# Kernel optimization log

Hardware: AMD Instinct MI355X
Metric: run time of the kernel (lower is better)

Reference implementation:

```python
import jax, jax.numpy as jnp
import numpy as np

B, T, I, H = 512, 256, 7, 64


def setup_inputs() -> dict:
    key = jax.random.key(0)
    d = {
        "x": jax.random.normal(jax.random.fold_in(key, 0), (B, T, I), jnp.float32),
        "C": jnp.zeros((B, H, H), jnp.float32),
        "n": jnp.zeros((B, H, H), jnp.float32),
    }
    for j, nm in enumerate(["Wq", "Wk", "Wv", "Wi", "Wf", "Wo"]):
        d[nm] = jax.random.normal(jax.random.fold_in(key, j + 1), (H, I), jnp.float32)
        d["b" + nm[1]] = jnp.zeros((H,), jnp.float32)
    return d


def reference(x, C, n, Wq, Wk, Wv, Wi, Wf, Wo, bq, bk, bv, bi, bf, bo):
    # x: [B,T,I]; C,n: [B,H,H] matrix memory / normalizer state
    Hdim = Wq.shape[0]
    scale = 1.0 / jnp.sqrt(jnp.asarray(Hdim, x.dtype))
    q = jnp.einsum('bti,hi->bth', x, Wq) + bq
    k = scale * (jnp.einsum('bti,hi->bth', x, Wk) + bk)
    v = jnp.einsum('bti,hi->bth', x, Wv) + bv
    i = jnp.exp(jnp.einsum('bti,hi->bth', x, Wi) + bi)
    f = jax.nn.sigmoid(jnp.einsum('bti,hi->bth', x, Wf) + bf)
    o = jax.nn.sigmoid(jnp.einsum('bti,hi->bth', x, Wo) + bo)
    # time-major for scan: each gate [T,B,H]
    gates = tuple(jnp.swapaxes(g, 0, 1) for g in (q, k, v, i, f, o))

    def step(carry, g):
        C, n = carry                      # [B,H,H]
        qt, kt, vt, it, ft, ot = g        # [B,H]
        ik = it * kt                      # [B,H]
        # torch: C = f*C + i*outer(v,k)  -> C[r,c] = f[c]*C[r,c] + i[c]*v[r]*k[c]
        C = ft[:, None, :] * C + ik[:, None, :] * vt[:, :, None]
        # torch: n = f*n + i*k (broadcast over rows)
        n = ft[:, None, :] * n + ik[:, None, :]
        num = jnp.einsum('brc,bc->br', C, qt)          # C @ q
        den = jnp.einsum('brc,br->bc', n, qt)          # n.T @ q
        h = ot * jnp.tanh(num / jnp.maximum(den, 1.0))
        return (C, n), h

    (C, n), hs = jax.lax.scan(step, (C, n), gates)
    return jnp.swapaxes(hs, 0, 1), C, n  # h: [B,T,H]
```

## Files before the change

### kernel.cpp

```cpp
#include <hip/hip_runtime.h>
#include <math.h>

#define B_ 512
#define T_ 256
#define I_ 7
#define H_ 64
#define L_ 16
#define NCH_ (T_ / L_)
#define L2E 1.44269504089f
#define GUARD2 (-21.64f)

typedef short bf16x8 __attribute__((ext_vector_type(8)));
typedef short short4v __attribute__((ext_vector_type(4)));
typedef float f32x4 __attribute__((ext_vector_type(4)));

__device__ __forceinline__ unsigned short f2bf(float f) {
  unsigned u = __float_as_uint(f);
  u += 0x7fff + ((u >> 16) & 1);
  return (unsigned short)(u >> 16);
}
__device__ __forceinline__ float ex2(float x) { return __builtin_amdgcn_exp2f(x); }
__device__ __forceinline__ float lg2(float x) { return __builtin_amdgcn_logf(x); }
__device__ __forceinline__ float logsig2(float a2) {
  return (a2 < GUARD2) ? a2 : -lg2(1.f + ex2(-a2));
}
__device__ __forceinline__ float sig2(float a2) {
  return __fdividef(1.f, 1.f + ex2(-a2));
}

#define PRODUCE_IKV(BUF, XP) do {                                             \
  float ls8[8], ik8[8];                                                       \
  unsigned short kv[8], vv[8];                                                \
  _Pragma("unroll") for (int tt = 0; tt < 8; ++tt) {                          \
    const int t = tb + tt;                                                    \
    float xs[7];                                                              \
    _Pragma("unroll") for (int jj = 0; jj < 7; ++jj) xs[jj] = (XP)[t * 7 + jj]; \
    float fp = bF2, ip = bI2, kp = bK, vp = bV;                               \
    _Pragma("unroll") for (int jj = 0; jj < 7; ++jj) {                        \
      fp = fmaf(xs[jj], wf2[jj], fp); ip = fmaf(xs[jj], wi2[jj], ip);         \
      kp = fmaf(xs[jj], wk[jj], kp);  vp = fmaf(xs[jj], wv[jj], vp);          \
    }                                                                         \
    ls8[tt] = logsig2(fp);                                                    \
    const float ikv = ex2(ip) * kp * 0.125f;                                  \
    ik8[tt] = ikv;                                                            \
    sIK[BUF][t][lane] = ikv;                                                  \
    vv[tt] = f2bf(vp);                                                        \
  }                                                                           \
  _Pragma("unroll") for (int tt = 1; tt < 8; ++tt) ls8[tt] += ls8[tt - 1];    \
  _Pragma("unroll") for (int tt = 0; tt < 8; ++tt) {                          \
    const float e = (tb == 0) ? (ls8[7] - ls8[tt]) : (-ls8[tt]);              \
    const float u = ik8[tt] * ex2(e);                                         \
    kv[tt] = f2bf(u);                                                         \
    sKt[BUF][tb + tt][lane] = kv[tt];                                         \
  }                                                                           \
  { short4v p0 = {(short)kv[0], (short)kv[1], (short)kv[2], (short)kv[3]};    \
    short4v p1 = {(short)kv[4], (short)kv[5], (short)kv[6], (short)kv[7]};    \
    *(short4v*)&sKnT[BUF][lane][tb]     = p0;                                 \
    *(short4v*)&sKnT[BUF][lane][tb + 4] = p1;                                 \
    short4v q0 = {(short)vv[0], (short)vv[1], (short)vv[2], (short)vv[3]};    \
    short4v q1 = {(short)vv[4], (short)vv[5], (short)vv[6], (short)vv[7]};    \
    *(short4v*)&sVT[BUF][lane][tb]     = q0;                                  \
    *(short4v*)&sVT[BUF][lane][tb + 4] = q1; }                                \
} while (0)

#define PRODUCE_F(BUF, XP) do {                                               \
  float ls[16];                                                               \
  _Pragma("unroll") for (int t = 0; t < 16; ++t) {                            \
    float xs[7];                                                              \
    _Pragma("unroll") for (int jj = 0; jj < 7; ++jj) xs[jj] = (XP)[t * 7 + jj]; \
    float fp = bF2;                                                           \
    _Pragma("unroll") for (int jj = 0; jj < 7; ++jj) fp = fmaf(xs[jj], wf2[jj], fp); \
    const float ena = ex2(-fp);                                               \
    sFs[BUF][t][lane] = __fdividef(1.f, 1.f + ena);                           \
    ls[t] = (fp < GUARD2) ? fp : -lg2(1.f + ena);                             \
  }                                                                           \
  _Pragma("unroll") for (int t = 1; t < 16; ++t) ls[t] += ls[t - 1];          \
  sEM[BUF][lane]   = ex2(ls[7]);                                              \
  sFtot[BUF][lane] = ex2(ls[15]);                                             \
  sCF[BUF][lane]   = ex2(ls[15] - ls[7]);                                     \
  { const int tq = lane & 15;                                                 \
    float Sqv = wqs[7];                                                       \
    _Pragma("unroll") for (int jj = 0; jj < 7; ++jj)                          \
      Sqv = fmaf((XP)[tq * 7 + jj], wqs[jj], Sqv);                            \
    if (lane < 16) sSq[BUF][tq] = Sqv; }                                      \
} while (0)

#define PRODUCE_Q(BUF, XP) do {                                               \
  float qv[16], ls[16];                                                       \
  _Pragma("unroll") for (int t = 0; t < 16; ++t) {                            \
    float xs[7];                                                              \
    _Pragma("unroll") for (int jj = 0; jj < 7; ++jj) xs[jj] = (XP)[t * 7 + jj]; \
    float qq = bQ, fp = bF2;                                                  \
    _Pragma("unroll") for (int jj = 0; jj < 7; ++jj) {                        \
      qq = fmaf(xs[jj], wq[jj], qq); fp = fmaf(xs[jj], wf2[jj], fp);          \
    }                                                                         \
    qv[t] = qq;                                                               \
    ls[t] = logsig2(fp);                                                      \
  }                                                                           \
  _Pragma("unroll") for (int t = 1; t < 16; ++t) ls[t] += ls[t - 1];          \
  const float m = ls[7];                                                      \
  _Pragma("unroll") for (int t = 0; t < 16; ++t)                              \
    sQt[BUF][t][lane] = f2bf(qv[t] * ex2(ls[t] - m));                         \
} while (0)

__global__ __launch_bounds__(512, 4) void mlstm_ws3(
    const float* __restrict__ x,
    const float* __restrict__ Cin,
    const float* __restrict__ nin,
    const float* __restrict__ Wq, const float* __restrict__ bq,
    const float* __restrict__ Wk, const float* __restrict__ bk,
    const float* __restrict__ Wv, const float* __restrict__ bv,
    const float* __restrict__ Wi, const float* __restrict__ bi,
    const float* __restrict__ Wf, const float* __restrict__ bf,
    const float* __restrict__ Wo, const float* __restrict__ bo,
    float* __restrict__ hout, float* __restrict__ Cout, float* __restrict__ nout)
{
  const int b    = blockIdx.x;
  const int tid  = threadIdx.x;
  const int lane = tid & 63;
  const int w    = __builtin_amdgcn_readfirstlane(tid >> 6);
  const int quad = lane >> 4;
  const int sl   = lane & 15;

  __shared__ __align__(16) unsigned short sQt[2][L_][72];
  __shared__ __align__(16) unsigned short sKt[2][L_][72];
  __shared__ __align__(16) unsigned short sVT[2][H_][40];
  __shared__ __align__(16) unsigned short sKnT[2][H_][40];
  __shared__ __align__(16) unsigned short sS[4][L_][40];
  __shared__ __align__(16) unsigned short sC0[H_][72];
  __shared__ float sFs[2][L_][H_];
  __shared__ float sIK[2][L_][H_];
  __shared__ float sSq[2][L_];
  __shared__ float sEM[2][H_];
  __shared__ float sFtot[2][H_];
  __shared__ float sCF[2][H_];
  __shared__ float sNv[H_];

  for (int idx = tid; idx < 1024; idx += 512) {
    const int bu = idx >> 9, r = (idx >> 3) & 63, d = idx & 7;
    ((unsigned*)sVT)[(bu * 64 + r) * 20 + 8 + d]  = 0;
    ((unsigned*)sKnT)[(bu * 64 + r) * 20 + 8 + d] = 0;
  }
  for (int idx = tid; idx < 1280; idx += 512) ((unsigned*)sS)[idx] = 0;

  const float* __restrict__ xb = x + (size_t)b * T_ * I_;

  if (w < 4) {
    const int c0 = 16 * w + sl;
    float wOl[7];
#pragma unroll
    for (int jj = 0; jj < 7; ++jj) wOl[jj] = Wo[c0 * 7 + jj] * L2E;
    const float bO2 = bo[c0] * L2E;
    f32x4 Cacc[4];
#pragma unroll
    for (int ct = 0; ct < 4; ++ct)
#pragma unroll
      for (int reg = 0; reg < 4; ++reg)
        Cacc[ct][reg] =
            Cin[(size_t)b * H_ * H_ + (size_t)(16 * w + 4 * quad + reg) * H_ + 16 * ct + sl];
    float nv = nin[(size_t)b * H_ * H_ + c0];
    __syncthreads();
    for (int j = 0; j < NCH_; ++j) {
      const int p = j & 1;
      const float* xc = xb + (size_t)j * L_ * I_;
      float den4[4];
#pragma unroll
      for (int t = 0; t < 16; ++t) {
        const float fs  = sFs[p][t][c0];
        const float ikv = sIK[p][t][c0];
        nv = fmaf(fs, nv, ikv);
        if ((t >> 2) == quad) den4[t & 3] = nv;
      }
      float idn[4], oo[4];
#pragma unroll
      for (int r2 = 0; r2 < 4; ++r2) {
        const int t = 4 * quad + r2;
        idn[r2] = __fdividef(1.f, fmaxf(den4[r2] * sSq[p][t], 1.f));
        float op = bO2;
#pragma unroll
        for (int jj = 0; jj < 7; ++jj) op = fmaf(xc[t * 7 + jj], wOl[jj], op);
        oo[r2] = sig2(op);
      }
      const bf16x8 aQ0 = *(const bf16x8*)&sQt[p][sl][8 * quad];
      const bf16x8 aQ1 = *(const bf16x8*)&sQt[p][sl][32 + 8 * quad];
      const bf16x8 bK0 = *(const bf16x8*)&sKt[p][sl][8 * quad];
      const bf16x8 bK1 = *(const bf16x8*)&sKt[p][sl][32 + 8 * quad];
      f32x4 Sv = {0.f, 0.f, 0.f, 0.f};
      Sv = __builtin_amdgcn_mfma_f32_16x16x32_bf16(aQ0, bK0, Sv, 0, 0, 0);
      Sv = __builtin_amdgcn_mfma_f32_16x16x32_bf16(aQ1, bK1, Sv, 0, 0, 0);
#pragma unroll
      for (int reg = 0; reg < 4; ++reg) {
        const int t = 4 * quad + reg;
        sS[w][t][sl] = f2bf((sl <= t) ? Sv[reg] : 0.f);
      }
      const bf16x8 aV = *(const bf16x8*)&sVT[p][c0][8 * quad];
      f32x4 G[4];
      float ftA[4], cfA[4];
#pragma unroll
      for (int ct = 0; ct < 4; ++ct) {
        const int cc = 16 * ct + sl;
        const float emv = sEM[p][cc];
        ftA[ct] = sFtot[p][cc];
        cfA[ct] = sCF[p][cc];
#pragma unroll
        for (int reg = 0; reg < 4; ++reg)
          sC0[16 * w + 4 * quad + reg][cc] = f2bf(Cacc[ct][reg] * emv);
        const bf16x8 bKn = *(const bf16x8*)&sKnT[p][cc][8 * quad];
        f32x4 z = {0.f, 0.f, 0.f, 0.f};
        G[ct] = __builtin_amdgcn_mfma_f32_16x16x32_bf16(aV, bKn, z, 0, 0, 0);
      }
      const bf16x8 bC0a = *(const bf16x8*)&sC0[c0][8 * quad];
      const bf16x8 bC0b = *(const bf16x8*)&sC0[c0][32 + 8 * quad];
      const bf16x8 aS   = *(const bf16x8*)&sS[w][sl][8 * quad];
      f32x4 Num = {0.f, 0.f, 0.f, 0.f};
      Num = __builtin_amdgcn_mfma_f32_16x16x32_bf16(aQ0, bC0a, Num, 0, 0, 0);
      Num = __builtin_amdgcn_mfma_f32_16x16x32_bf16(aQ1, bC0b, Num, 0, 0, 0);
      Num = __builtin_amdgcn_mfma_f32_16x16x32_bf16(aS, aV, Num, 0, 0, 0);
#pragma unroll
      for (int reg = 0; reg < 4; ++reg) {
        const int t = 4 * quad + reg;
        const float y = Num[reg] * idn[reg];
        const float e = ex2(y * 2.88539008178f);
        const float th = 1.f - __fdividef(2.f, e + 1.f);
        hout[(size_t)b * T_ * H_ + (size_t)(j * L_ + t) * H_ + c0] = oo[reg] * th;
      }
#pragma unroll
      for (int ct = 0; ct < 4; ++ct) Cacc[ct] = Cacc[ct] * ftA[ct] + G[ct] * cfA[ct];
      __syncthreads();
    }
#pragma unroll
    for (int ct = 0; ct < 4; ++ct)
#pragma unroll
      for (int reg = 0; reg < 4; ++reg)
        Cout[(size_t)b * H_ * H_ + (size_t)(16 * w + 4 * quad + reg) * H_ + 16 * ct + sl] =
            Cacc[ct][reg];
    if (quad == 0) sNv[c0] = nv;
  } else if (w == 4 || w == 5) {
    const int tb = (w == 4) ? 0 : 8;
    float wi2[7], wk[7], wf2[7], wv[7];
#pragma unroll
    for (int jj = 0; jj < 7; ++jj) {
      wi2[jj] = Wi[lane * 7 + jj] * L2E;
      wk[jj]  = Wk[lane * 7 + jj];
      wf2[jj] = Wf[lane * 7 + jj] * L2E;
      wv[jj]  = Wv[lane * 7 + jj];
    }
    const float bI2 = bi[lane] * L2E, bK = bk[lane], bF2 = bf[lane] * L2E, bV = bv[lane];
    PRODUCE_IKV(0, xb);
    __syncthreads();
    for (int j = 0; j < NCH_; ++j) {
      if (j + 1 < NCH_) {
        const int pn = (j + 1) & 1;
        const float* xn = xb + (size_t)(j + 1) * L_ * I_;
        if (pn) PRODUCE_IKV(1, xn); else PRODUCE_IKV(0, xn);
      }
      __syncthreads();
    }
  } else if (w == 6) {
    float wf2[7], wqs[8];
#pragma unroll
    for (int jj = 0; jj < 7; ++jj) wf2[jj] = Wf[lane * 7 + jj] * L2E;
    const float bF2 = bf[lane] * L2E;
#pragma unroll
    for (int jj = 0; jj < 7; ++jj) {
      float s = 0.f;
      for (int r = 0; r < H_; ++r) s += Wq[r * 7 + jj];
      wqs[jj] = s;
    }
    {
      float s = 0.f;
      for (int r = 0; r < H_; ++r) s += bq[r];
      wqs[7] = s;
    }
    PRODUCE_F(0, xb);
    __syncthreads();
    for (int j = 0; j < NCH_; ++j) {
      if (j + 1 < NCH_) {
        const int pn = (j + 1) & 1;
        const float* xn = xb + (size_t)(j + 1) * L_ * I_;
        if (pn) PRODUCE_F(1, xn); else PRODUCE_F(0, xn);
      }
      __syncthreads();
    }
  } else {
    float wq[7], wf2[7];
#pragma unroll
    for (int jj = 0; jj < 7; ++jj) {
      wq[jj]  = Wq[lane * 7 + jj];
      wf2[jj] = Wf[lane * 7 + jj] * L2E;
    }
    const float bQ = bq[lane], bF2 = bf[lane] * L2E;
    PRODUCE_Q(0, xb);
    __syncthreads();
    for (int j = 0; j < NCH_; ++j) {
      if (j + 1 < NCH_) {
        const int pn = (j + 1) & 1;
        const float* xn = xb + (size_t)(j + 1) * L_ * I_;
        if (pn) PRODUCE_Q(1, xn); else PRODUCE_Q(0, xn);
      }
      __syncthreads();
    }
  }

  __syncthreads();
  {
    const float nvv = sNv[lane];
#pragma unroll
    for (int k = 0; k < 8; ++k)
      nout[(size_t)b * H_ * H_ + (size_t)(8 * w + k) * H_ + lane] = nvv;
  }
}

extern "C" void kernel_launch(void* const* d_in, const int* in_sizes, int n_in,
                              void* d_out, int out_size, void* d_ws, size_t ws_size,
                              hipStream_t stream) {
  const float* xp  = (const float*)d_in[0];
  const float* Cp  = (const float*)d_in[1];
  const float* np_ = (const float*)d_in[2];

  const float* W[6];
  const float* Bv[6];
  if (n_in >= 15 && in_sizes[4] == 64) {
    for (int g = 0; g < 6; ++g) {
      W[g]  = (const float*)d_in[3 + 2 * g];
      Bv[g] = (const float*)d_in[4 + 2 * g];
    }
  } else {
    for (int g = 0; g < 6; ++g) {
      W[g]  = (const float*)d_in[3 + g];
      Bv[g] = (const float*)d_in[9 + g];
    }
  }

  float* hout = (float*)d_out;
  float* Cout = hout + (size_t)B_ * T_ * H_;
  float* nout = Cout + (size_t)B_ * H_ * H_;

  mlstm_ws3<<<dim3(B_), dim3(512), 0, stream>>>(
      xp, Cp, np_,
      W[0], Bv[0], W[1], Bv[1], W[2], Bv[2],
      W[3], Bv[3], W[4], Bv[4], W[5], Bv[5],
      hout, Cout, nout);
}
```

Before: 155.4 us.

## Split each batch across two row-half blocks with fewer producer warps

Each batch element now runs as two 256-thread blocks that each own 32 rows of the C state, which doubles the grid and shrinks per-block shared memory. The producer roles are consolidated: one warp computes i, k and f plus the decay factors, and another computes q together with the summed q row. V projection moves into the consumer warps, and the forget gate is rebuilt from stored log-sigmoids. Each half-block recomputes the full k/f/q projections, so that work is duplicated in exchange for more parallelism and occupancy.

```diff
diff --git a/kernel.cpp b/kernel.cpp
--- a/kernel.cpp
+++ b/kernel.cpp
@@ -28,82 +28,79 @@
   return __fdividef(1.f, 1.f + ex2(-a2));
 }
 
-#define PRODUCE_IKV(BUF, XP) do {                                             \
-  float ls8[8], ik8[8];                                                       \
-  unsigned short kv[8], vv[8];                                                \
-  _Pragma("unroll") for (int tt = 0; tt < 8; ++tt) {                          \
-    const int t = tb + tt;                                                    \
-    float xs[7];                                                              \
-    _Pragma("unroll") for (int jj = 0; jj < 7; ++jj) xs[jj] = (XP)[t * 7 + jj]; \
-    float fp = bF2, ip = bI2, kp = bK, vp = bV;                               \
-    _Pragma("unroll") for (int jj = 0; jj < 7; ++jj) {                        \
-      fp = fmaf(xs[jj], wf2[jj], fp); ip = fmaf(xs[jj], wi2[jj], ip);         \
-      kp = fmaf(xs[jj], wk[jj], kp);  vp = fmaf(xs[jj], wv[jj], vp);          \
-    }                                                                         \
-    ls8[tt] = logsig2(fp);                                                    \
-    const float ikv = ex2(ip) * kp * 0.125f;                                  \
-    ik8[tt] = ikv;                                                            \
-    sIK[BUF][t][lane] = ikv;                                                  \
-    vv[tt] = f2bf(vp);                                                        \
-  }                                                                           \
-  _Pragma("unroll") for (int tt = 1; tt < 8; ++tt) ls8[tt] += ls8[tt - 1];    \
-  _Pragma("unroll") for (int tt = 0; tt < 8; ++tt) {                          \
-    const float e = (tb == 0) ? (ls8[7] - ls8[tt]) : (-ls8[tt]);              \
-    const float u = ik8[tt] * ex2(e);                                         \
-    kv[tt] = f2bf(u);                                                         \
-    sKt[BUF][tb + tt][lane] = kv[tt];                                         \
-  }                                                                           \
-  { short4v p0 = {(short)kv[0], (short)kv[1], (short)kv[2], (short)kv[3]};    \
-    short4v p1 = {(short)kv[4], (short)kv[5], (short)kv[6], (short)kv[7]};    \
-    *(short4v*)&sKnT[BUF][lane][tb]     = p0;                                 \
-    *(short4v*)&sKnT[BUF][lane][tb + 4] = p1;                                 \
-    short4v q0 = {(short)vv[0], (short)vv[1], (short)vv[2], (short)vv[3]};    \
-    short4v q1 = {(short)vv[4], (short)vv[5], (short)vv[6], (short)vv[7]};    \
-    *(short4v*)&sVT[BUF][lane][tb]     = q0;                                  \
-    *(short4v*)&sVT[BUF][lane][tb + 4] = q1; }                                \
+#define CONS_V(BUF, XP) do {                                                  \
+  unsigned short vv[4];                                                       \
+  _Pragma("unroll") for (int i2 = 0; i2 < 4; ++i2) {                          \
+    const int t = 4 * quad + i2;                                              \
+    float vp = bV;                                                            \
+    _Pragma("unroll") for (int jj = 0; jj < 7; ++jj)                          \
+      vp = fmaf((XP)[t * 7 + jj], wVl[jj], vp);                               \
+    vv[i2] = f2bf(vp);                                                        \
+  }                                                                           \
+  short4v pk = {(short)vv[0], (short)vv[1], (short)vv[2], (short)vv[3]};      \
+  *(short4v*)&sVT[BUF][16 * w + sl][4 * quad] = pk;                           \
 } while (0)
 
-#define PRODUCE_F(BUF, XP) do {                                               \
-  float ls[16];                                                               \
+#define PROD_IKF(BUF, XP) do {                                                \
+  float cl[16], ikv[16];                                                      \
   _Pragma("unroll") for (int t = 0; t < 16; ++t) {                            \
     float xs[7];                                                              \
     _Pragma("unroll") for (int jj = 0; jj < 7; ++jj) xs[jj] = (XP)[t * 7 + jj]; \
-    float fp = bF2;                                                           \
-    _Pragma("unroll") for (int jj = 0; jj < 7; ++jj) fp = fmaf(xs[jj], wf2[jj], fp); \
-    const float ena = ex2(-fp);                                               \
-    sFs[BUF][t][lane] = __fdividef(1.f, 1.f + ena);                           \
-    ls[t] = (fp < GUARD2) ? fp : -lg2(1.f + ena);                             \
-  }                                                                           \
-  _Pragma("unroll") for (int t = 1; t < 16; ++t) ls[t] += ls[t - 1];          \
-  sEM[BUF][lane]   = ex2(ls[7]);                                              \
-  sFtot[BUF][lane] = ex2(ls[15]);                                             \
-  sCF[BUF][lane]   = ex2(ls[15] - ls[7]);                                     \
-  { const int tq = lane & 15;                                                 \
-    float Sqv = wqs[7];                                                       \
-    _Pragma("unroll") for (int jj = 0; jj < 7; ++jj)                          \
-      Sqv = fmaf((XP)[tq * 7 + jj], wqs[jj], Sqv);                            \
-    if (lane < 16) sSq[BUF][tq] = Sqv; }                                      \
+    float fp = bF2, ip = bI2, kp = bK;                                        \
+    _Pragma("unroll") for (int jj = 0; jj < 7; ++jj) {                        \
+      fp = fmaf(xs[jj], wf2[jj], fp);                                         \
+      ip = fmaf(xs[jj], wi2[jj], ip);                                         \
+      kp = fmaf(xs[jj], wk[jj], kp);                                          \
+    }                                                                         \
+    const float ls = logsig2(fp);                                             \
+    cl[t] = ls;                                                               \
+    const float ik = ex2(ip) * kp * 0.125f;                                   \
+    ikv[t] = ik;                                                              \
+    if (oh) { sIK[BUF][t][lc2] = ik; sLs[BUF][t][lc2] = ls; }                 \
+  }                                                                           \
+  _Pragma("unroll") for (int t = 1; t < 16; ++t) cl[t] += cl[t - 1];          \
+  const float m = cl[7];                                                      \
+  sEM[BUF][lane] = ex2(m);                                                    \
+  sCF[BUF][lane] = ex2(cl[15] - m);                                           \
+  unsigned short kvv[16];                                                     \
+  _Pragma("unroll") for (int t = 0; t < 16; ++t) {                            \
+    const float u = ikv[t] * ex2(m - cl[t]);                                  \
+    kvv[t] = f2bf(u);                                                         \
+    sKt[BUF][t][lane] = kvv[t];                                               \
+  }                                                                           \
+  _Pragma("unroll") for (int g = 0; g < 4; ++g) {                             \
+    short4v pk = {(short)kvv[4 * g], (short)kvv[4 * g + 1],                   \
+                  (short)kvv[4 * g + 2], (short)kvv[4 * g + 3]};              \
+    *(short4v*)&sKnT[BUF][lane][4 * g] = pk;                                  \
+  }                                                                           \
 } while (0)
 
-#define PRODUCE_Q(BUF, XP) do {                                               \
-  float qv[16], ls[16];                                                       \
+#define PROD_Q(BUF, XP) do {                                                  \
+  float qv[16], cl[16];                                                       \
   _Pragma("unroll") for (int t = 0; t < 16; ++t) {                            \
     float xs[7];                                                              \
     _Pragma("unroll") for (int jj = 0; jj < 7; ++jj) xs[jj] = (XP)[t * 7 + jj]; \
     float qq = bQ, fp = bF2;                                                  \
     _Pragma("unroll") for (int jj = 0; jj < 7; ++jj) {                        \
-      qq = fmaf(xs[jj], wq[jj], qq); fp = fmaf(xs[jj], wf2[jj], fp);          \
+      qq = fmaf(xs[jj], wq[jj], qq);                                          \
+      fp = fmaf(xs[jj], wf2[jj], fp);                                         \
     }                                                                         \
     qv[t] = qq;                                                               \
-    ls[t] = logsig2(fp);                                                      \
-  }                                                                           \
-  _Pragma("unroll") for (int t = 1; t < 16; ++t) ls[t] += ls[t - 1];          \
-  const float m = ls[7];                                                      \
+    cl[t] = logsig2(fp);                                                      \
+  }                                                                           \
+  _Pragma("unroll") for (int t = 1; t < 16; ++t) cl[t] += cl[t - 1];          \
+  const float m = cl[7];                                                      \
   _Pragma("unroll") for (int t = 0; t < 16; ++t)                              \
-    sQt[BUF][t][lane] = f2bf(qv[t] * ex2(ls[t] - m));                         \
+    sQt[BUF][t][lane] = f2bf(qv[t] * ex2(cl[t] - m));                         \
+  if (lane < 16) {                                                            \
+    float Sqv = wqs[7];                                                       \
+    _Pragma("unroll") for (int jj = 0; jj < 7; ++jj)                          \
+      Sqv = fmaf((XP)[lane * 7 + jj], wqs[jj], Sqv);                          \
+    sSq[BUF][lane] = Sqv;                                                     \
+  }                                                                           \
 } while (0)
 
-__global__ __launch_bounds__(512, 4) void mlstm_ws3(
+__global__ __launch_bounds__(256, 4) void mlstm_rs(
     const float* __restrict__ x,
     const float* __restrict__ Cin,
     const float* __restrict__ nin,
@@ -115,7 +112,10 @@
     const float* __restrict__ Wo, const float* __restrict__ bo,
     float* __restrict__ hout, float* __restrict__ Cout, float* __restrict__ nout)
 {
-  const int b    = blockIdx.x;
+  const int bb   = blockIdx.x;
+  const int b    = bb >> 1;
+  const int half = bb & 1;
+  const int rbase = half << 5;
   const int tid  = threadIdx.x;
   const int lane = tid & 63;
   const int w    = __builtin_amdgcn_readfirstlane(tid >> 6);
@@ -124,62 +124,59 @@
 
   __shared__ __align__(16) unsigned short sQt[2][L_][72];
   __shared__ __align__(16) unsigned short sKt[2][L_][72];
-  __shared__ __align__(16) unsigned short sVT[2][H_][40];
   __shared__ __align__(16) unsigned short sKnT[2][H_][40];
-  __shared__ __align__(16) unsigned short sS[4][L_][40];
-  __shared__ __align__(16) unsigned short sC0[H_][72];
-  __shared__ float sFs[2][L_][H_];
-  __shared__ float sIK[2][L_][H_];
+  __shared__ __align__(16) unsigned short sVT[2][32][40];
+  __shared__ __align__(16) unsigned short sS[2][L_][32];
+  __shared__ __align__(16) unsigned short sC0[32][72];
+  __shared__ float sLs[2][L_][32];
+  __shared__ float sIK[2][L_][32];
   __shared__ float sSq[2][L_];
   __shared__ float sEM[2][H_];
-  __shared__ float sFtot[2][H_];
   __shared__ float sCF[2][H_];
-  __shared__ float sNv[H_];
-
-  for (int idx = tid; idx < 1024; idx += 512) {
-    const int bu = idx >> 9, r = (idx >> 3) & 63, d = idx & 7;
-    ((unsigned*)sVT)[(bu * 64 + r) * 20 + 8 + d]  = 0;
-    ((unsigned*)sKnT)[(bu * 64 + r) * 20 + 8 + d] = 0;
-  }
-  for (int idx = tid; idx < 1280; idx += 512) ((unsigned*)sS)[idx] = 0;
+  __shared__ float sNv[32];
+
+  for (int idx = tid; idx < 1024; idx += 256) {
+    const int r = idx >> 3, d = idx & 7;
+    ((unsigned*)sKnT)[r * 20 + 8 + d] = 0;
+  }
+  for (int idx = tid; idx < 512; idx += 256) {
+    const int r = idx >> 3, d = idx & 7;
+    ((unsigned*)sVT)[r * 20 + 8 + d] = 0;
+  }
+  for (int idx = tid; idx < 512; idx += 256) ((unsigned*)sS)[idx] = 0;
 
   const float* __restrict__ xb = x + (size_t)b * T_ * I_;
 
-  if (w < 4) {
-    const int c0 = 16 * w + sl;
-    float wOl[7];
-#pragma unroll
-    for (int jj = 0; jj < 7; ++jj) wOl[jj] = Wo[c0 * 7 + jj] * L2E;
-    const float bO2 = bo[c0] * L2E;
+  if (w < 2) {
+    const int lc  = 16 * w + sl;
+    const int c0g = rbase + lc;
+    float wOl[7], wVl[7];
+#pragma unroll
+    for (int jj = 0; jj < 7; ++jj) {
+      wOl[jj] = Wo[c0g * 7 + jj] * L2E;
+      wVl[jj] = Wv[c0g * 7 + jj];
+    }
+    const float bO2 = bo[c0g] * L2E, bV = bv[c0g];
     f32x4 Cacc[4];
 #pragma unroll
     for (int ct = 0; ct < 4; ++ct)
 #pragma unroll
       for (int reg = 0; reg < 4; ++reg)
-        Cacc[ct][reg] =
-            Cin[(size_t)b * H_ * H_ + (size_t)(16 * w + 4 * quad + reg) * H_ + 16 * ct + sl];
-    float nv = nin[(size_t)b * H_ * H_ + c0];
+        Cacc[ct][reg] = Cin[(size_t)b * H_ * H_ +
+                            (size_t)(rbase + 16 * w + 4 * quad + reg) * H_ + 16 * ct + sl];
+    float nv = nin[(size_t)b * H_ * H_ + c0g];
+    CONS_V(0, xb);
     __syncthreads();
     for (int j = 0; j < NCH_; ++j) {
-      const int p = j & 1;
+      const int p = j & 1, pn = p ^ 1;
       const float* xc = xb + (size_t)j * L_ * I_;
+      const float* xn = xc + L_ * I_;
       float den4[4];
 #pragma unroll
       for (int t = 0; t < 16; ++t) {
-        const float fs  = sFs[p][t][c0];
-        const float ikv = sIK[p][t][c0];
-        nv = fmaf(fs, nv, ikv);
+        const float fs = ex2(sLs[p][t][lc]);
+        nv = fmaf(fs, nv, sIK[p][t][lc]);
         if ((t >> 2) == quad) den4[t & 3] = nv;
-      }
-      float idn[4], oo[4];
-#pragma unroll
-      for (int r2 = 0; r2 < 4; ++r2) {
-        const int t = 4 * quad + r2;
-        idn[r2] = __fdividef(1.f, fmaxf(den4[r2] * sSq[p][t], 1.f));
-        float op = bO2;
-#pragma unroll
-        for (int jj = 0; jj < 7; ++jj) op = fmaf(xc[t * 7 + jj], wOl[jj], op);
-        oo[r2] = sig2(op);
       }
       const bf16x8 aQ0 = *(const bf16x8*)&sQt[p][sl][8 * quad];
       const bf16x8 aQ1 = *(const bf16x8*)&sQt[p][sl][32 + 8 * quad];
@@ -188,20 +185,30 @@
       f32x4 Sv = {0.f, 0.f, 0.f, 0.f};
       Sv = __builtin_amdgcn_mfma_f32_16x16x32_bf16(aQ0, bK0, Sv, 0, 0, 0);
       Sv = __builtin_amdgcn_mfma_f32_16x16x32_bf16(aQ1, bK1, Sv, 0, 0, 0);
+      float idn[4], oo[4];
+#pragma unroll
+      for (int r2 = 0; r2 < 4; ++r2) {
+        const int t = 4 * quad + r2;
+        idn[r2] = __fdividef(1.f, fmaxf(den4[r2] * sSq[p][t], 1.f));
+        float op = bO2;
+#pragma unroll
+        for (int jj = 0; jj < 7; ++jj) op = fmaf(xc[t * 7 + jj], wOl[jj], op);
+        oo[r2] = sig2(op);
+      }
 #pragma unroll
       for (int reg = 0; reg < 4; ++reg) {
         const int t = 4 * quad + reg;
         sS[w][t][sl] = f2bf((sl <= t) ? Sv[reg] : 0.f);
       }
-      const bf16x8 aV = *(const bf16x8*)&sVT[p][c0][8 * quad];
+      const bf16x8 aV = *(const bf16x8*)&sVT[p][16 * w + sl][8 * quad];
       f32x4 G[4];
       float ftA[4], cfA[4];
 #pragma unroll
       for (int ct = 0; ct < 4; ++ct) {
         const int cc = 16 * ct + sl;
         const float emv = sEM[p][cc];
-        ftA[ct] = sFtot[p][cc];
         cfA[ct] = sCF[p][cc];
+        ftA[ct] = emv * cfA[ct];
 #pragma unroll
         for (int reg = 0; reg < 4; ++reg)
           sC0[16 * w + 4 * quad + reg][cc] = f2bf(Cacc[ct][reg] * emv);
@@ -209,8 +216,9 @@
         f32x4 z = {0.f, 0.f, 0.f, 0.f};
         G[ct] = __builtin_amdgcn_mfma_f32_16x16x32_bf16(aV, bKn, z, 0, 0, 0);
       }
-      const bf16x8 bC0a = *(const bf16x8*)&sC0[c0][8 * quad];
-      const bf16x8 bC0b = *(const bf16x8*)&sC0[c0][32 + 8 * quad];
+      if (j + 1 < NCH_) CONS_V(pn, xn);
+      const bf16x8 bC0a = *(const bf16x8*)&sC0[16 * w + sl][8 * quad];
+      const bf16x8 bC0b = *(const bf16x8*)&sC0[16 * w + sl][32 + 8 * quad];
       const bf16x8 aS   = *(const bf16x8*)&sS[w][sl][8 * quad];
       f32x4 Num = {0.f, 0.f, 0.f, 0.f};
       Num = __builtin_amdgcn_mfma_f32_16x16x32_bf16(aQ0, bC0a, Num, 0, 0, 0);
@@ -222,7 +230,7 @@
         const float y = Num[reg] * idn[reg];
         const float e = ex2(y * 2.88539008178f);
         const float th = 1.f - __fdividef(2.f, e + 1.f);
-        hout[(size_t)b * T_ * H_ + (size_t)(j * L_ + t) * H_ + c0] = oo[reg] * th;
+        hout[(size_t)b * T_ * H_ + (size_t)(j * L_ + t) * H_ + c0g] = oo[reg] * th;
       }
 #pragma unroll
       for (int ct = 0; ct < 4; ++ct) Cacc[ct] = Cacc[ct] * ftA[ct] + G[ct] * cfA[ct];
@@ -232,82 +240,70 @@
     for (int ct = 0; ct < 4; ++ct)
 #pragma unroll
       for (int reg = 0; reg < 4; ++reg)
-        Cout[(size_t)b * H_ * H_ + (size_t)(16 * w + 4 * quad + reg) * H_ + 16 * ct + sl] =
-            Cacc[ct][reg];
-    if (quad == 0) sNv[c0] = nv;
-  } else if (w == 4 || w == 5) {
-    const int tb = (w == 4) ? 0 : 8;
-    float wi2[7], wk[7], wf2[7], wv[7];
+        Cout[(size_t)b * H_ * H_ +
+             (size_t)(rbase + 16 * w + 4 * quad + reg) * H_ + 16 * ct + sl] = Cacc[ct][reg];
+    if (quad == 0) sNv[lc] = nv;
+  } else if (w == 2) {
+    float wi2[7], wk[7], wf2[7];
 #pragma unroll
     for (int jj = 0; jj < 7; ++jj) {
       wi2[jj] = Wi[lane * 7 + jj] * L2E;
       wk[jj]  = Wk[lane * 7 + jj];
       wf2[jj] = Wf[lane * 7 + jj] * L2E;
-      wv[jj]  = Wv[lane * 7 + jj];
-    }
-    const float bI2 = bi[lane] * L2E, bK = bk[lane], bF2 = bf[lane] * L2E, bV = bv[lane];
-    PRODUCE_IKV(0, xb);
+    }
+    const float bI2 = bi[lane] * L2E, bK = bk[lane], bF2 = bf[lane] * L2E;
+    const int oh  = ((lane >> 5) == half);
+    const int lc2 = lane & 31;
+    PROD_IKF(0, xb);
     __syncthreads();
     for (int j = 0; j < NCH_; ++j) {
       if (j + 1 < NCH_) {
         const int pn = (j + 1) & 1;
         const float* xn = xb + (size_t)(j + 1) * L_ * I_;
-        if (pn) PRODUCE_IKV(1, xn); else PRODUCE_IKV(0, xn);
+        PROD_IKF(pn, xn);
       }
       __syncthreads();
     }
-  } else if (w == 6) {
-    float wf2[7], wqs[8];
-#pragma unroll
-    for (int jj = 0; jj < 7; ++jj) wf2[jj] = Wf[lane * 7 + jj] * L2E;
-    const float bF2 = bf[lane] * L2E;
+  } else {
+    float wq[7], wf2[7];
 #pragma unroll
     for (int jj = 0; jj < 7; ++jj) {
-      float s = 0.f;
-      for (int r = 0; r < H_; ++r) s += Wq[r * 7 + jj];
+      wq[jj]  = Wq[lane * 7 + jj];
+      wf2[jj] = Wf[lane * 7 + jj] * L2E;
+    }
+    const float bQ = bq[lane], bF2 = bf[lane] * L2E;
+    float wqs[8];
+#pragma unroll
+    for (int jj = 0; jj < 7; ++jj) {
+      float s = wq[jj];
+#pragma unroll
+      for (int off = 32; off >= 1; off >>= 1) s += __shfl_xor(s, off);
       wqs[jj] = s;
     }
     {
-      float s = 0.f;
-      for (int r = 0; r < H_; ++r) s += bq[r];
+      float s = bQ;
+#pragma unroll
+      for (int off = 32; off >= 1; off >>= 1) s += __shfl_xor(s, off);
       wqs[7] = s;
     }
-    PRODUCE_F(0, xb);
+    PROD_Q(0, xb);
     __syncthreads();
     for (int j = 0; j < NCH_; ++j) {
       if (j + 1 < NCH_) {
         const int pn = (j + 1) & 1;
         const float* xn = xb + (size_t)(j + 1) * L_ * I_;
-        if (pn) PRODUCE_F(1, xn); else PRODUCE_F(0, xn);
+        PROD_Q(pn, xn);
       }
       __syncthreads();
     }
-  } else {
-    float wq[7], wf2[7];
-#pragma unroll
-    for (int jj = 0; jj < 7; ++jj) {
-      wq[jj]  = Wq[lane * 7 + jj];
-      wf2[jj] = Wf[lane * 7 + jj] * L2E;
-    }
-    const float bQ = bq[lane], bF2 = bf[lane] * L2E;
-    PRODUCE_Q(0, xb);
-    __syncthreads();
-    for (int j = 0; j < NCH_; ++j) {
-      if (j + 1 < NCH_) {
-        const int pn = (j + 1) & 1;
-        const float* xn = xb + (size_t)(j + 1) * L_ * I_;
-        if (pn) PRODUCE_Q(1, xn); else PRODUCE_Q(0, xn);
-      }
-      __syncthreads();
-    }
   }
 
   __syncthreads();
-  {
-    const float nvv = sNv[lane];
-#pragma unroll
-    for (int k = 0; k < 8; ++k)
-      nout[(size_t)b * H_ * H_ + (size_t)(8 * w + k) * H_ + lane] = nvv;
+#pragma unroll
+  for (int k = 0; k < 8; ++k) {
+    const int idx = tid * 8 + k;
+    const int r = idx >> 5, cl2 = idx & 31;
+    nout[(size_t)b * H_ * H_ + (size_t)r * H_ + rbase + cl2] = sNv[cl2];
   }
 }
 
@@ -336,7 +332,7 @@
   float* Cout = hout + (size_t)B_ * T_ * H_;
   float* nout = Cout + (size_t)B_ * H_ * H_;
 
-  mlstm_ws3<<<dim3(B_), dim3(512), 0, stream>>>(
+  mlstm_rs<<<dim3(B_ * 2), dim3(256), 0, stream>>>(
       xp, Cp, np_,
       W[0], Bv[0], W[1], Bv[1], W[2], Bv[2],
       W[3], Bv[3], W[4], Bv[4], W[5], Bv[5],
```

Result: slower. 284.4 us (+83.0%).

## Restructure warp-specialized producer pipeline to offload normalizer and gates from MFMA warps

Applied to the files above, without the earlier changes.

Reorganizes the producer warps into a deeper software pipeline. Warp 6 computes log-sigmoid forget prefixes two chunks ahead, warps 4-5 split i*k and exp-scaled k/v work across stages, and warp 7 now runs the normalizer recurrence, inverse denominators and output-gate preactivations. The MFMA consumer warps no longer run the serial n recurrence or the o-gate dot products. They fold the C update into the MFMA accumulator by scaling k with the total forget factor. The costs are more shared memory, triple-buffered sEM/sFtot, bf16 storage of the o preactivation with some precision loss, and more complex cross-stage dependencies.

```diff
diff --git a/kernel.cpp b/kernel.cpp
--- a/kernel.cpp
+++ b/kernel.cpp
@@ -19,6 +19,9 @@
   u += 0x7fff + ((u >> 16) & 1);
   return (unsigned short)(u >> 16);
 }
+__device__ __forceinline__ float bf2f(unsigned short u) {
+  return __uint_as_float(((unsigned)u) << 16);
+}
 __device__ __forceinline__ float ex2(float x) { return __builtin_amdgcn_exp2f(x); }
 __device__ __forceinline__ float lg2(float x) { return __builtin_amdgcn_logf(x); }
 __device__ __forceinline__ float logsig2(float a2) {
@@ -28,82 +31,99 @@
   return __fdividef(1.f, 1.f + ex2(-a2));
 }
 
-#define PRODUCE_IKV(BUF, XP) do {                                             \
-  float ls8[8], ik8[8];                                                       \
-  unsigned short kv[8], vv[8];                                                \
+#define DO_PRE(C) do {                                                        \
+  const float* xp_ = xb + (C) * (L_ * I_);                                    \
   _Pragma("unroll") for (int tt = 0; tt < 8; ++tt) {                          \
     const int t = tb + tt;                                                    \
     float xs[7];                                                              \
-    _Pragma("unroll") for (int jj = 0; jj < 7; ++jj) xs[jj] = (XP)[t * 7 + jj]; \
-    float fp = bF2, ip = bI2, kp = bK, vp = bV;                               \
+    _Pragma("unroll") for (int jj = 0; jj < 7; ++jj) xs[jj] = xp_[t * 7 + jj];\
+    float ip = bI2, kp = bK;                                                  \
     _Pragma("unroll") for (int jj = 0; jj < 7; ++jj) {                        \
-      fp = fmaf(xs[jj], wf2[jj], fp); ip = fmaf(xs[jj], wi2[jj], ip);         \
-      kp = fmaf(xs[jj], wk[jj], kp);  vp = fmaf(xs[jj], wv[jj], vp);          \
+      ip = fmaf(xs[jj], wi2[jj], ip);                                         \
+      kp = fmaf(xs[jj], wk[jj], kp);                                          \
     }                                                                         \
-    ls8[tt] = logsig2(fp);                                                    \
-    const float ikv = ex2(ip) * kp * 0.125f;                                  \
-    ik8[tt] = ikv;                                                            \
-    sIK[BUF][t][lane] = ikv;                                                  \
+    const float ik = ex2(ip) * kp * 0.125f;                                   \
+    ik8[tt] = ik;                                                             \
+    sIK[(C) & 1][t][lane] = ik;                                               \
+  }                                                                           \
+} while (0)
+
+#define DO_EXPV(C) do {                                                       \
+  const float* xp_ = xb + (C) * (L_ * I_);                                    \
+  float lsv[16];                                                              \
+  _Pragma("unroll") for (int t = 0; t < 16; ++t) lsv[t] = sLs[(C) & 1][lane][t]; \
+  _Pragma("unroll") for (int t = 1; t < 16; ++t) lsv[t] += lsv[t - 1];        \
+  const float m = lsv[7];                                                     \
+  const float scl = ex2(lsv[15] - m);                                         \
+  unsigned short kh[8], vv[8];                                                \
+  _Pragma("unroll") for (int tt = 0; tt < 8; ++tt) {                          \
+    const int t = tb + tt;                                                    \
+    const float u = ik8[tt] * ex2(m - lsv[t]);                                \
+    sKt[(C) & 1][t][lane] = f2bf(u);                                          \
+    kh[tt] = f2bf(u * scl);                                                   \
+    float vp = bV;                                                            \
+    _Pragma("unroll") for (int jj = 0; jj < 7; ++jj)                          \
+      vp = fmaf(xp_[t * 7 + jj], wv[jj], vp);                                 \
     vv[tt] = f2bf(vp);                                                        \
   }                                                                           \
-  _Pragma("unroll") for (int tt = 1; tt < 8; ++tt) ls8[tt] += ls8[tt - 1];    \
-  _Pragma("unroll") for (int tt = 0; tt < 8; ++tt) {                          \
-    const float e = (tb == 0) ? (ls8[7] - ls8[tt]) : (-ls8[tt]);              \
-    const float u = ik8[tt] * ex2(e);                                         \
-    kv[tt] = f2bf(u);                                                         \
-    sKt[BUF][tb + tt][lane] = kv[tt];                                         \
-  }                                                                           \
-  { short4v p0 = {(short)kv[0], (short)kv[1], (short)kv[2], (short)kv[3]};    \
-    short4v p1 = {(short)kv[4], (short)kv[5], (short)kv[6], (short)kv[7]};    \
-    *(short4v*)&sKnT[BUF][lane][tb]     = p0;                                 \
-    *(short4v*)&sKnT[BUF][lane][tb + 4] = p1;                                 \
+  { short4v p0 = {(short)kh[0], (short)kh[1], (short)kh[2], (short)kh[3]};    \
+    short4v p1 = {(short)kh[4], (short)kh[5], (short)kh[6], (short)kh[7]};    \
+    *(short4v*)&sKnT[(C) & 1][lane][tb]     = p0;                             \
+    *(short4v*)&sKnT[(C) & 1][lane][tb + 4] = p1;                             \
     short4v q0 = {(short)vv[0], (short)vv[1], (short)vv[2], (short)vv[3]};    \
     short4v q1 = {(short)vv[4], (short)vv[5], (short)vv[6], (short)vv[7]};    \
-    *(short4v*)&sVT[BUF][lane][tb]     = q0;                                  \
-    *(short4v*)&sVT[BUF][lane][tb + 4] = q1; }                                \
+    *(short4v*)&sVT[(C) & 1][lane][tb]     = q0;                              \
+    *(short4v*)&sVT[(C) & 1][lane][tb + 4] = q1; }                            \
 } while (0)
 
-#define PRODUCE_F(BUF, XP) do {                                               \
+#define DO_F(C) do {                                                          \
+  const float* xp_ = xb + (C) * (L_ * I_);                                    \
   float ls[16];                                                               \
   _Pragma("unroll") for (int t = 0; t < 16; ++t) {                            \
-    float xs[7];                                                              \
-    _Pragma("unroll") for (int jj = 0; jj < 7; ++jj) xs[jj] = (XP)[t * 7 + jj]; \
     float fp = bF2;                                                           \
-    _Pragma("unroll") for (int jj = 0; jj < 7; ++jj) fp = fmaf(xs[jj], wf2[jj], fp); \
-    const float ena = ex2(-fp);                                               \
-    sFs[BUF][t][lane] = __fdividef(1.f, 1.f + ena);                           \
-    ls[t] = (fp < GUARD2) ? fp : -lg2(1.f + ena);                             \
+    _Pragma("unroll") for (int jj = 0; jj < 7; ++jj)                          \
+      fp = fmaf(xp_[t * 7 + jj], wf2[jj], fp);                                \
+    ls[t] = logsig2(fp);                                                      \
+    sLs[(C) & 1][lane][t] = ls[t];                                            \
   }                                                                           \
   _Pragma("unroll") for (int t = 1; t < 16; ++t) ls[t] += ls[t - 1];          \
-  sEM[BUF][lane]   = ex2(ls[7]);                                              \
-  sFtot[BUF][lane] = ex2(ls[15]);                                             \
-  sCF[BUF][lane]   = ex2(ls[15] - ls[7]);                                     \
-  { const int tq = lane & 15;                                                 \
+  sEM[(C) % 3][lane]   = ex2(ls[7]);                                          \
+  sFtot[(C) % 3][lane] = ex2(ls[15]);                                         \
+  if (lane < 16) {                                                            \
     float Sqv = wqs[7];                                                       \
     _Pragma("unroll") for (int jj = 0; jj < 7; ++jj)                          \
-      Sqv = fmaf((XP)[tq * 7 + jj], wqs[jj], Sqv);                            \
-    if (lane < 16) sSq[BUF][tq] = Sqv; }                                      \
+      Sqv = fmaf(xp_[lane * 7 + jj], wqs[jj], Sqv);                           \
+    sSq[(C) & 1][lane] = Sqv;                                                 \
+  }                                                                           \
 } while (0)
 
-#define PRODUCE_Q(BUF, XP) do {                                               \
-  float qv[16], ls[16];                                                       \
+#define DO_W7(C) do {                                                         \
+  const float* xp_ = xb + (C) * (L_ * I_);                                    \
+  float lsv[16];                                                              \
   _Pragma("unroll") for (int t = 0; t < 16; ++t) {                            \
-    float xs[7];                                                              \
-    _Pragma("unroll") for (int jj = 0; jj < 7; ++jj) xs[jj] = (XP)[t * 7 + jj]; \
-    float qq = bQ, fp = bF2;                                                  \
+    lsv[t] = sLs[(C) & 1][lane][t];                                           \
+    const float fs = ex2(lsv[t]);                                             \
+    nv = fmaf(fs, nv, sIK[(C) & 1][t][lane]);                                 \
+    sInvDen[(C) & 1][t][lane] =                                               \
+        __fdividef(1.f, fmaxf(nv * sSq[(C) & 1][t], 1.f));                    \
+  }                                                                           \
+  float qv[16];                                                               \
+  _Pragma("unroll") for (int t = 0; t < 16; ++t) {                            \
+    float qq = bQ, op = bO2;                                                  \
     _Pragma("unroll") for (int jj = 0; jj < 7; ++jj) {                        \
-      qq = fmaf(xs[jj], wq[jj], qq); fp = fmaf(xs[jj], wf2[jj], fp);          \
+      qq = fmaf(xp_[t * 7 + jj], wq[jj], qq);                                 \
+      op = fmaf(xp_[t * 7 + jj], wo2[jj], op);                                \
     }                                                                         \
     qv[t] = qq;                                                               \
-    ls[t] = logsig2(fp);                                                      \
-  }                                                                           \
-  _Pragma("unroll") for (int t = 1; t < 16; ++t) ls[t] += ls[t - 1];          \
-  const float m = ls[7];                                                      \
+    sOpre[(C) & 1][t][lane] = f2bf(op);                                       \
+  }                                                                           \
+  _Pragma("unroll") for (int t = 1; t < 16; ++t) lsv[t] += lsv[t - 1];        \
+  const float m = lsv[7];                                                     \
   _Pragma("unroll") for (int t = 0; t < 16; ++t)                              \
-    sQt[BUF][t][lane] = f2bf(qv[t] * ex2(ls[t] - m));                         \
+    sQt[(C) & 1][t][lane] = f2bf(qv[t] * ex2(lsv[t] - m));                    \
 } while (0)
 
-__global__ __launch_bounds__(512, 4) void mlstm_ws3(
+__global__ __launch_bounds__(512, 4) void mlstm_u(
     const float* __restrict__ x,
     const float* __restrict__ Cin,
     const float* __restrict__ nin,
@@ -121,66 +141,98 @@
   const int w    = __builtin_amdgcn_readfirstlane(tid >> 6);
   const int quad = lane >> 4;
   const int sl   = lane & 15;
+  const int c0   = 16 * (w & 3) + sl;
 
   __shared__ __align__(16) unsigned short sQt[2][L_][72];
   __shared__ __align__(16) unsigned short sKt[2][L_][72];
+  __shared__ __align__(16) unsigned short sKnT[2][H_][40];
   __shared__ __align__(16) unsigned short sVT[2][H_][40];
-  __shared__ __align__(16) unsigned short sKnT[2][H_][40];
-  __shared__ __align__(16) unsigned short sS[4][L_][40];
+  __shared__ __align__(16) unsigned short sS[4][L_][32];
   __shared__ __align__(16) unsigned short sC0[H_][72];
-  __shared__ float sFs[2][L_][H_];
+  __shared__ __align__(16) unsigned short sOpre[2][L_][72];
+  __shared__ float sInvDen[2][L_][68];
   __shared__ float sIK[2][L_][H_];
+  __shared__ float sLs[2][H_][17];
   __shared__ float sSq[2][L_];
-  __shared__ float sEM[2][H_];
-  __shared__ float sFtot[2][H_];
-  __shared__ float sCF[2][H_];
+  __shared__ float sEM[3][H_];
+  __shared__ float sFtot[3][H_];
   __shared__ float sNv[H_];
 
   for (int idx = tid; idx < 1024; idx += 512) {
-    const int bu = idx >> 9, r = (idx >> 3) & 63, d = idx & 7;
-    ((unsigned*)sVT)[(bu * 64 + r) * 20 + 8 + d]  = 0;
-    ((unsigned*)sKnT)[(bu * 64 + r) * 20 + 8 + d] = 0;
-  }
-  for (int idx = tid; idx < 1280; idx += 512) ((unsigned*)sS)[idx] = 0;
+    const int r = idx >> 3, d = idx & 7;
+    ((unsigned*)sKnT)[r * 20 + 8 + d] = 0;
+    ((unsigned*)sVT)[r * 20 + 8 + d]  = 0;
+  }
+  for (int idx = tid; idx < 1024; idx += 512) ((unsigned*)sS)[idx] = 0;
 
   const float* __restrict__ xb = x + (size_t)b * T_ * I_;
 
+  f32x4 Cacc[4];
+  float wi2[7], wk[7], wv[7], ik8[8];
+  float bI2 = 0.f, bK = 0.f, bV = 0.f;
+  int tb = 0;
+  float wf2[7], wqs[8];
+  float bF2 = 0.f;
+  float wq[7], wo2[7];
+  float bQ = 0.f, bO2 = 0.f, nv = 0.f;
+
   if (w < 4) {
-    const int c0 = 16 * w + sl;
-    float wOl[7];
-#pragma unroll
-    for (int jj = 0; jj < 7; ++jj) wOl[jj] = Wo[c0 * 7 + jj] * L2E;
-    const float bO2 = bo[c0] * L2E;
-    f32x4 Cacc[4];
 #pragma unroll
     for (int ct = 0; ct < 4; ++ct)
 #pragma unroll
       for (int reg = 0; reg < 4; ++reg)
         Cacc[ct][reg] =
             Cin[(size_t)b * H_ * H_ + (size_t)(16 * w + 4 * quad + reg) * H_ + 16 * ct + sl];
-    float nv = nin[(size_t)b * H_ * H_ + c0];
-    __syncthreads();
-    for (int j = 0; j < NCH_; ++j) {
-      const int p = j & 1;
-      const float* xc = xb + (size_t)j * L_ * I_;
-      float den4[4];
-#pragma unroll
-      for (int t = 0; t < 16; ++t) {
-        const float fs  = sFs[p][t][c0];
-        const float ikv = sIK[p][t][c0];
-        nv = fmaf(fs, nv, ikv);
-        if ((t >> 2) == quad) den4[t & 3] = nv;
-      }
-      float idn[4], oo[4];
-#pragma unroll
-      for (int r2 = 0; r2 < 4; ++r2) {
-        const int t = 4 * quad + r2;
-        idn[r2] = __fdividef(1.f, fmaxf(den4[r2] * sSq[p][t], 1.f));
-        float op = bO2;
-#pragma unroll
-        for (int jj = 0; jj < 7; ++jj) op = fmaf(xc[t * 7 + jj], wOl[jj], op);
-        oo[r2] = sig2(op);
-      }
+  } else if (w < 6) {
+    tb = (w == 4) ? 0 : 8;
+#pragma unroll
+    for (int jj = 0; jj < 7; ++jj) {
+      wi2[jj] = Wi[lane * 7 + jj] * L2E;
+      wk[jj]  = Wk[lane * 7 + jj];
+      wv[jj]  = Wv[lane * 7 + jj];
+    }
+    bI2 = bi[lane] * L2E; bK = bk[lane]; bV = bv[lane];
+  } else if (w == 6) {
+#pragma unroll
+    for (int jj = 0; jj < 7; ++jj) wf2[jj] = Wf[lane * 7 + jj] * L2E;
+    bF2 = bf[lane] * L2E;
+#pragma unroll
+    for (int jj = 0; jj < 7; ++jj) {
+      float s = Wq[lane * 7 + jj];
+#pragma unroll
+      for (int off = 32; off >= 1; off >>= 1) s += __shfl_xor(s, off);
+      wqs[jj] = s;
+    }
+    {
+      float s = bq[lane];
+#pragma unroll
+      for (int off = 32; off >= 1; off >>= 1) s += __shfl_xor(s, off);
+      wqs[7] = s;
+    }
+  } else {
+#pragma unroll
+    for (int jj = 0; jj < 7; ++jj) {
+      wq[jj]  = Wq[lane * 7 + jj];
+      wo2[jj] = Wo[lane * 7 + jj] * L2E;
+    }
+    bQ = bq[lane]; bO2 = bo[lane] * L2E;
+    nv = nin[(size_t)b * H_ * H_ + lane];
+  }
+
+  if (w == 4 || w == 5) DO_PRE(0);
+  else if (w == 6) DO_F(0);
+  __syncthreads();
+
+  if (w == 4 || w == 5) { DO_EXPV(0); DO_PRE(1); }
+  else if (w == 6) DO_F(1);
+  else if (w == 7) DO_W7(0);
+  __syncthreads();
+
+#pragma unroll 1
+  for (int j = 0; j < NCH_; ++j) {
+    if (w < 4) {
+      const int p  = j & 1;
+      const int e3 = j % 3;
       const bf16x8 aQ0 = *(const bf16x8*)&sQt[p][sl][8 * quad];
       const bf16x8 aQ1 = *(const bf16x8*)&sQt[p][sl][32 + 8 * quad];
       const bf16x8 bK0 = *(const bf16x8*)&sKt[p][sl][8 * quad];
@@ -194,20 +246,17 @@
         sS[w][t][sl] = f2bf((sl <= t) ? Sv[reg] : 0.f);
       }
       const bf16x8 aV = *(const bf16x8*)&sVT[p][c0][8 * quad];
-      f32x4 G[4];
-      float ftA[4], cfA[4];
 #pragma unroll
       for (int ct = 0; ct < 4; ++ct) {
         const int cc = 16 * ct + sl;
-        const float emv = sEM[p][cc];
-        ftA[ct] = sFtot[p][cc];
-        cfA[ct] = sCF[p][cc];
+        const float em = sEM[e3][cc];
+        const float ft = sFtot[e3][cc];
 #pragma unroll
         for (int reg = 0; reg < 4; ++reg)
-          sC0[16 * w + 4 * quad + reg][cc] = f2bf(Cacc[ct][reg] * emv);
-        const bf16x8 bKn = *(const bf16x8*)&sKnT[p][cc][8 * quad];
-        f32x4 z = {0.f, 0.f, 0.f, 0.f};
-        G[ct] = __builtin_amdgcn_mfma_f32_16x16x32_bf16(aV, bKn, z, 0, 0, 0);
+          sC0[16 * w + 4 * quad + reg][cc] = f2bf(Cacc[ct][reg] * em);
+        Cacc[ct] *= ft;
+        const bf16x8 bH = *(const bf16x8*)&sKnT[p][cc][8 * quad];
+        Cacc[ct] = __builtin_amdgcn_mfma_f32_16x16x32_bf16(aV, bH, Cacc[ct], 0, 0, 0);
       }
       const bf16x8 bC0a = *(const bf16x8*)&sC0[c0][8 * quad];
       const bf16x8 bC0b = *(const bf16x8*)&sC0[c0][32 + 8 * quad];
@@ -219,89 +268,34 @@
 #pragma unroll
       for (int reg = 0; reg < 4; ++reg) {
         const int t = 4 * quad + reg;
-        const float y = Num[reg] * idn[reg];
+        const float o   = sig2(bf2f(sOpre[p][t][c0]));
+        const float idn = sInvDen[p][t][c0];
+        const float y = Num[reg] * idn;
         const float e = ex2(y * 2.88539008178f);
         const float th = 1.f - __fdividef(2.f, e + 1.f);
-        hout[(size_t)b * T_ * H_ + (size_t)(j * L_ + t) * H_ + c0] = oo[reg] * th;
+        hout[(size_t)b * T_ * H_ + (size_t)(j * L_ + t) * H_ + c0] = o * th;
       }
-#pragma unroll
-      for (int ct = 0; ct < 4; ++ct) Cacc[ct] = Cacc[ct] * ftA[ct] + G[ct] * cfA[ct];
-      __syncthreads();
-    }
+    } else if (w < 6) {
+      if (j + 1 < NCH_) DO_EXPV(j + 1);
+      if (j + 2 < NCH_) DO_PRE(j + 2);
+    } else if (w == 6) {
+      if (j + 2 < NCH_) DO_F(j + 2);
+    } else {
+      if (j + 1 < NCH_) DO_W7(j + 1);
+    }
+    __syncthreads();
+  }
+
+  if (w < 4) {
 #pragma unroll
     for (int ct = 0; ct < 4; ++ct)
 #pragma unroll
       for (int reg = 0; reg < 4; ++reg)
         Cout[(size_t)b * H_ * H_ + (size_t)(16 * w + 4 * quad + reg) * H_ + 16 * ct + sl] =
             Cacc[ct][reg];
-    if (quad == 0) sNv[c0] = nv;
-  } else if (w == 4 || w == 5) {
-    const int tb = (w == 4) ? 0 : 8;
-    float wi2[7], wk[7], wf2[7], wv[7];
-#pragma unroll
-    for (int jj = 0; jj < 7; ++jj) {
-      wi2[jj] = Wi[lane * 7 + jj] * L2E;
-      wk[jj]  = Wk[lane * 7 + jj];
-      wf2[jj] = Wf[lane * 7 + jj] * L2E;
-      wv[jj]  = Wv[lane * 7 + jj];
-    }
-    const float bI2 = bi[lane] * L2E, bK = bk[lane], bF2 = bf[lane] * L2E, bV = bv[lane];
-    PRODUCE_IKV(0, xb);
-    __syncthreads();
-    for (int j = 0; j < NCH_; ++j) {
-      if (j + 1 < NCH_) {
-        const int pn = (j + 1) & 1;
-        const float* xn = xb + (size_t)(j + 1) * L_ * I_;
-        if (pn) PRODUCE_IKV(1, xn); else PRODUCE_IKV(0, xn);
-      }
-      __syncthreads();
-    }
-  } else if (w == 6) {
-    float wf2[7], wqs[8];
-#pragma unroll
-    for (int jj = 0; jj < 7; ++jj) wf2[jj] = Wf[lane * 7 + jj] * L2E;
-    const float bF2 = bf[lane] * L2E;
-#pragma unroll
-    for (int jj = 0; jj < 7; ++jj) {
-      float s = 0.f;
-      for (int r = 0; r < H_; ++r) s += Wq[r * 7 + jj];
-      wqs[jj] = s;
-    }
-    {
-      float s = 0.f;
-      for (int r = 0; r < H_; ++r) s += bq[r];
-      wqs[7] = s;
-    }
-    PRODUCE_F(0, xb);
-    __syncthreads();
-    for (int j = 0; j < NCH_; ++j) {
-      if (j + 1 < NCH_) {
-        const int pn = (j + 1) & 1;
-        const float* xn = xb + (size_t)(j + 1) * L_ * I_;
-        if (pn) PRODUCE_F(1, xn); else PRODUCE_F(0, xn);
-      }
-      __syncthreads();
-    }
-  } else {
-    float wq[7], wf2[7];
-#pragma unroll
-    for (int jj = 0; jj < 7; ++jj) {
-      wq[jj]  = Wq[lane * 7 + jj];
-      wf2[jj] = Wf[lane * 7 + jj] * L2E;
-    }
-    const float bQ = bq[lane], bF2 = bf[lane] * L2E;
-    PRODUCE_Q(0, xb);
-    __syncthreads();
-    for (int j = 0; j < NCH_; ++j) {
-      if (j + 1 < NCH_) {
-        const int pn = (j + 1) & 1;
-        const float* xn = xb + (size_t)(j + 1) * L_ * I_;
-        if (pn) PRODUCE_Q(1, xn); else PRODUCE_Q(0, xn);
-      }
-      __syncthreads();
-    }
-  }
-
+  } else if (w == 7) {
+    sNv[lane] = nv;
+  }
   __syncthreads();
   {
     const float nvv = sNv[lane];
@@ -336,7 +330,7 @@
   float* Cout = hout + (size_t)B_ * T_ * H_;
   float* nout = Cout + (size_t)B_ * H_ * H_;
 
-  mlstm_ws3<<<dim3(B_), dim3(512), 0, stream>>>(
+  mlstm_u<<<dim3(B_), dim3(512), 0, stream>>>(
       xp, Cp, np_,
       W[0], Bv[0], W[1], Bv[1], W[2], Bv[2],
       W[3], Bv[3], W[4], Bv[4], W[5], Bv[5],
```

Result: slower. 177.8 us (+14.5%).
